# Kernel tuning notes

Hardware: AMD Instinct MI355X
Metric: run time of the kernel (lower is better)

## Reference

```python
import jax, jax.numpy as jnp
import numpy as np

N, NFEAT, OUT, NREL = 4096, 128, 64, 7


def setup_inputs() -> dict:
    key = jax.random.key(0)
    ks = jax.random.split(key, 12)
    mask = jax.random.uniform(ks[0], (NREL, N, N)) < 0.01
    vals = jax.random.uniform(ks[1], (NREL, N, N))
    A_stack = jnp.where(mask, vals, 0.0).astype(jnp.float32)
    feature = jax.random.normal(ks[2], (N, NFEAT), jnp.float32)
    encode = (jax.random.uniform(ks[3], (N, NREL)) < 0.3).astype(jnp.float32)
    stdv = 1.0 / np.sqrt(OUT)
    W1 = jax.random.uniform(ks[4], (NFEAT, OUT), jnp.float32, -stdv, stdv)
    b1 = jax.random.uniform(ks[5], (OUT,), jnp.float32, -stdv, stdv)
    W2 = jax.random.uniform(ks[6], (OUT, OUT), jnp.float32, -stdv, stdv)
    b2 = jax.random.uniform(ks[7], (OUT,), jnp.float32, -stdv, stdv)
    weight_b = jax.random.uniform(ks[8], (NREL, 1), jnp.float32, 0.0, 0.1)
    relation_interaction = 0.1 * jax.random.normal(ks[9], (3, 3), jnp.float32)
    interaction_strength = jnp.array([0.5], jnp.float32)
    struct_weight = jax.random.uniform(ks[10], (NREL,), jnp.float32, 0.0, 0.1)
    return dict(feature=feature, A_stack=A_stack, encode=encode, W1=W1, b1=b1,
                W2=W2, b2=b2, weight_b=weight_b,
                relation_interaction=relation_interaction,
                interaction_strength=interaction_strength,
                struct_weight=struct_weight)


def _l2_normalize(x):
    norm = jnp.clip(jnp.linalg.norm(x, axis=1, keepdims=True), 1e-12)
    return x / norm


def _gcn(x, adj, W, b):
    # torch.mm(input, weight) then torch.spmm(adj, support) + bias
    return adj @ (x @ W) + b


def reference(feature, A_stack, encode, W1, b1, W2, b2, weight_b,
              relation_interaction, interaction_strength, struct_weight):
    # adj_matrix_weight_merge: weighted sum of 7 relation adjacencies, symmetrized
    merged = jnp.einsum('rnm,r->nm', A_stack, weight_b[:, 0])  # [N,N]
    bbp_A = merged + merged.T

    # relation-interaction enhancement over the first 3 relations (i != j)
    R = A_stack[:3]  # [3,N,N]
    M = relation_interaction * (1.0 - jnp.eye(3, dtype=relation_interaction.dtype))
    mult = jnp.einsum('ij,inm,jnm->nm', M, R, R)                       # coeff*Ri*Rj
    cond = jnp.einsum('ij,inm,jnm->nm', M, (R > 0).astype(R.dtype), R)  # coeff*(Ri>0)*Rj
    interaction_A = jnp.tanh(0.6 * mult + 0.4 * cond)

    final_A = bbp_A + interaction_strength[0] * interaction_A

    U1 = _gcn(feature, final_A, W1, b1)
    U2 = _gcn(U1, final_A, W2, b2)

    # construct_adj(encode, struct_weight): weighted structural similarity
    struct_adj = (encode * struct_weight) @ encode.T  # [N,N]
    U3 = _gcn(feature, struct_adj, W1, b1)
    U4 = _gcn(U3, struct_adj, W2, b2)

    branch1 = (U1 + U2) / 2
    result = (branch1 + U4) / 2
    branch2 = U4
    return (_l2_normalize(result), _l2_normalize(branch1), _l2_normalize(branch2))
```

## Files before the change

kernel.cpp:

```cpp
#include <hip/hip_runtime.h>
#include <math.h>

#define NDIM 4096
#define NNSZ ((size_t)NDIM*(size_t)NDIM)
#define SCAP 262144u

typedef __attribute__((ext_vector_type(8))) short short8;
typedef __attribute__((ext_vector_type(4))) float f32x4;

__device__ __forceinline__ unsigned short f2bf(float x) {
  unsigned u = __float_as_uint(x);
  u += 0x7FFFu + ((u >> 16) & 1u);
  return (unsigned short)(u >> 16);
}
__device__ __forceinline__ float bf2f(unsigned short u) {
  return __uint_as_float(((unsigned)u) << 16);
}

__device__ __forceinline__ float inter_term(float r0, float r1, float r2,
    float m01, float m02, float m10, float m12, float m20, float m21) {
  float mult = (m01 + m10) * (r0 * r1) + (m02 + m20) * (r0 * r2) + (m12 + m21) * (r1 * r2);
  float i0 = (r0 > 0.f) ? 1.f : 0.f;
  float i1 = (r1 > 0.f) ? 1.f : 0.f;
  float i2 = (r2 > 0.f) ? 1.f : 0.f;
  float cond = m01 * i0 * r1 + m02 * i0 * r2
             + m10 * i1 * r0 + m12 * i1 * r2
             + m20 * i2 * r0 + m21 * i2 * r1;
  float a = 0.6f * mult + 0.4f * cond;
  return (a == 0.0f) ? 0.0f : tanhf(a);
}

__global__ __launch_bounds__(256, 4) void k_pass1(
    const float* __restrict__ A, const float* __restrict__ wb,
    const float* __restrict__ Mri, const float* __restrict__ strength,
    unsigned short* __restrict__ Mm, unsigned* __restrict__ sidx,
    float* __restrict__ sval, unsigned* __restrict__ scnt)
{
  const unsigned gid = blockIdx.x * 256 + threadIdx.x;
  const size_t off = (size_t)gid * 4;

  float w[7];
#pragma unroll
  for (int r = 0; r < 7; ++r) w[r] = wb[r];
  const float m01 = Mri[1], m02 = Mri[2], m10 = Mri[3];
  const float m12 = Mri[5], m20 = Mri[6], m21 = Mri[7];
  const float s = strength[0];

  float4 v[7];
#pragma unroll
  for (int r = 0; r < 7; ++r)
    v[r] = *(const float4*)(A + (size_t)r * NNSZ + off);

  float4 acc = make_float4(0.f, 0.f, 0.f, 0.f);
#pragma unroll
  for (int r = 0; r < 7; ++r) {
    acc.x = fmaf(w[r], v[r].x, acc.x);
    acc.y = fmaf(w[r], v[r].y, acc.y);
    acc.z = fmaf(w[r], v[r].z, acc.z);
    acc.w = fmaf(w[r], v[r].w, acc.w);
  }
  *(ushort4*)(Mm + off) = make_ushort4(f2bf(acc.x), f2bf(acc.y), f2bf(acc.z), f2bf(acc.w));

  {
    float r0 = v[0].x, r1 = v[1].x, r2 = v[2].x;
    if ((int)(r0 != 0.f) + (int)(r1 != 0.f) + (int)(r2 != 0.f) >= 2) {
      float t = inter_term(r0, r1, r2, m01, m02, m10, m12, m20, m21);
      unsigned idx = atomicAdd(scnt, 1u);
      if (idx < SCAP) { sidx[idx] = (unsigned)(off + 0); sval[idx] = s * t; }
    }
  }
  {
    float r0 = v[0].y, r1 = v[1].y, r2 = v[2].y;
    if ((int)(r0 != 0.f) + (int)(r1 != 0.f) + (int)(r2 != 0.f) >= 2) {
      float t = inter_term(r0, r1, r2, m01, m02, m10, m12, m20, m21);
      unsigned idx = atomicAdd(scnt, 1u);
      if (idx < SCAP) { sidx[idx] = (unsigned)(off + 1); sval[idx] = s * t; }
    }
  }
  {
    float r0 = v[0].z, r1 = v[1].z, r2 = v[2].z;
    if ((int)(r0 != 0.f) + (int)(r1 != 0.f) + (int)(r2 != 0.f) >= 2) {
      float t = inter_term(r0, r1, r2, m01, m02, m10, m12, m20, m21);
      unsigned idx = atomicAdd(scnt, 1u);
      if (idx < SCAP) { sidx[idx] = (unsigned)(off + 2); sval[idx] = s * t; }
    }
  }
  {
    float r0 = v[0].w, r1 = v[1].w, r2 = v[2].w;
    if ((int)(r0 != 0.f) + (int)(r1 != 0.f) + (int)(r2 != 0.f) >= 2) {
      float t = inter_term(r0, r1, r2, m01, m02, m10, m12, m20, m21);
      unsigned idx = atomicAdd(scnt, 1u);
      if (idx < SCAP) { sidx[idx] = (unsigned)(off + 3); sval[idx] = s * t; }
    }
  }
}

__global__ __launch_bounds__(256) void k_pass2(
    const unsigned short* __restrict__ Mm, unsigned short* __restrict__ F)
{
  const int bi = blockIdx.x, bj = blockIdx.y;
  __shared__ unsigned short t[64 * 65];
  const int x  = threadIdx.x >> 2;
  const int y0 = (threadIdx.x & 3) << 4;

  const size_t moff = (size_t)(bj * 64 + x) * NDIM + bi * 64 + y0;
  unsigned short mv[16];
  ((uint4*)mv)[0] = *(const uint4*)(Mm + moff);
  ((uint4*)mv)[1] = *(const uint4*)(Mm + moff + 8);
#pragma unroll
  for (int e = 0; e < 16; ++e) t[x * 65 + y0 + e] = mv[e];
  __syncthreads();

  const size_t off = (size_t)(bi * 64 + x) * NDIM + bj * 64 + y0;
  unsigned short pv[16], ov[16];
  ((uint4*)pv)[0] = *(const uint4*)(Mm + off);
  ((uint4*)pv)[1] = *(const uint4*)(Mm + off + 8);
#pragma unroll
  for (int e = 0; e < 16; ++e)
    ov[e] = f2bf(bf2f(pv[e]) + bf2f(t[(y0 + e) * 65 + x]));
  *(uint4*)(F + off)     = ((const uint4*)ov)[0];
  *(uint4*)(F + off + 8) = ((const uint4*)ov)[1];
}

__global__ __launch_bounds__(256) void k_fix(const unsigned* __restrict__ sidx,
    const float* __restrict__ sval, const unsigned* __restrict__ scnt,
    unsigned short* __restrict__ F) {
  unsigned n = *scnt;
  if (n > SCAP) n = SCAP;
  for (unsigned i = blockIdx.x * 256 + threadIdx.x; i < n; i += gridDim.x * 256) {
    unsigned pos = sidx[i];
    F[pos] = f2bf(bf2f(F[pos]) + sval[i]);
  }
}

__global__ __launch_bounds__(64) void k_z1(const float* __restrict__ feat,
    const float* __restrict__ W1, float* __restrict__ Z1) {
  int n = blockIdx.x, j = threadIdx.x;
  __shared__ float fr[128];
  fr[j] = feat[n * 128 + j];
  fr[j + 64] = feat[n * 128 + 64 + j];
  __syncthreads();
  float acc = 0.f;
#pragma unroll 8
  for (int k = 0; k < 128; ++k) acc = fmaf(fr[k], W1[k * 64 + j], acc);
  Z1[(size_t)n * 64 + j] = acc;
}

__global__ __launch_bounds__(256) void k_transpose_bf16(
    const float* __restrict__ Z, unsigned short* __restrict__ Zt) {
  __shared__ float tile[64][65];
  const int n0 = blockIdx.x * 64;
  const int c = threadIdx.x & 63;
  const int r0 = threadIdx.x >> 6;
#pragma unroll
  for (int i = 0; i < 16; ++i) {
    int r = r0 * 16 + i;
    tile[r][c] = Z[(size_t)(n0 + r) * 64 + c];
  }
  __syncthreads();
#pragma unroll
  for (int i = 0; i < 16; ++i) {
    int j = r0 * 16 + i;
    Zt[(size_t)j * NDIM + n0 + c] = f2bf(tile[c][j]);
  }
}

__global__ __launch_bounds__(512) void k_mfma_gemm(
    const unsigned short* __restrict__ Fb,
    const unsigned short* __restrict__ Zt,
    const float* __restrict__ bias,
    float* __restrict__ U)
{
  __shared__ float red[8][16][66];
  const int strip = blockIdx.x * 16;
  const int w = threadIdx.x >> 6;
  const int lane = threadIdx.x & 63;
  const int arow = lane & 15;
  const int kq = lane >> 4;
  const int k_base = w * 512;

  f32x4 acc[4] = {};
  const unsigned short* Ap  = Fb + (size_t)(strip + arow) * NDIM + k_base + kq * 8;
  const unsigned short* Bp0 = Zt + (size_t)(arow) * NDIM + k_base + kq * 8;
  const unsigned short* Bp1 = Bp0 + (size_t)16 * NDIM;
  const unsigned short* Bp2 = Bp0 + (size_t)32 * NDIM;
  const unsigned short* Bp3 = Bp0 + (size_t)48 * NDIM;

#pragma unroll 4
  for (int step = 0; step < 16; ++step) {
    const int k0 = step * 32;
    short8 a  = *(const short8*)(Ap  + k0);
    short8 b0 = *(const short8*)(Bp0 + k0);
    short8 b1v = *(const short8*)(Bp1 + k0);
    short8 b2v = *(const short8*)(Bp2 + k0);
    short8 b3v = *(const short8*)(Bp3 + k0);
    acc[0] = __builtin_amdgcn_mfma_f32_16x16x32_bf16(a, b0,  acc[0], 0, 0, 0);
    acc[1] = __builtin_amdgcn_mfma_f32_16x16x32_bf16(a, b1v, acc[1], 0, 0, 0);
    acc[2] = __builtin_amdgcn_mfma_f32_16x16x32_bf16(a, b2v, acc[2], 0, 0, 0);
    acc[3] = __builtin_amdgcn_mfma_f32_16x16x32_bf16(a, b3v, acc[3], 0, 0, 0);
  }
#pragma unroll
  for (int t = 0; t < 4; ++t)
#pragma unroll
    for (int r = 0; r < 4; ++r)
      red[w][kq * 4 + r][t * 16 + arow] = acc[t][r];
  __syncthreads();

  const int col = threadIdx.x & 63;
  const int row0 = threadIdx.x >> 6;
#pragma unroll
  for (int rr = 0; rr < 2; ++rr) {
    const int row = row0 + rr * 8;
    float sum = 0.f;
#pragma unroll
    for (int ww = 0; ww < 8; ++ww) sum += red[ww][row][col];
    U[(size_t)(strip + row) * 64 + col] = sum + bias[col];
  }
}

__device__ __forceinline__ float wave_sum64(float v) {
#pragma unroll
  for (int o = 32; o > 0; o >>= 1) v += __shfl_xor(v, o, 64);
  return v;
}

__global__ __launch_bounds__(512) void k_gemm2f(
    const unsigned short* __restrict__ Fb,
    const unsigned short* __restrict__ Zt,
    const float* __restrict__ b2,
    const float* __restrict__ U1,
    const float* __restrict__ encode,
    const float* __restrict__ sw,
    const float* __restrict__ G2,
    float* __restrict__ out)
{
  __shared__ float red[8][16][66];
  const int strip = blockIdx.x * 16;
  const int w = threadIdx.x >> 6;
  const int lane = threadIdx.x & 63;
  const int arow = lane & 15;
  const int kq = lane >> 4;
  const int k_base = w * 512;

  f32x4 acc[4] = {};
  const unsigned short* Ap  = Fb + (size_t)(strip + arow) * NDIM + k_base + kq * 8;
  const unsigned short* Bp0 = Zt + (size_t)(arow) * NDIM + k_base + kq * 8;
  const unsigned short* Bp1 = Bp0 + (size_t)16 * NDIM;
  const unsigned short* Bp2 = Bp0 + (size_t)32 * NDIM;
  const unsigned short* Bp3 = Bp0 + (size_t)48 * NDIM;

#pragma unroll 4
  for (int step = 0; step < 16; ++step) {
    const int k0 = step * 32;
    short8 a  = *(const short8*)(Ap  + k0);
    short8 b0 = *(const short8*)(Bp0 + k0);
    short8 b1v = *(const short8*)(Bp1 + k0);
    short8 b2v = *(const short8*)(Bp2 + k0);
    short8 b3v = *(const short8*)(Bp3 + k0);
    acc[0] = __builtin_amdgcn_mfma_f32_16x16x32_bf16(a, b0,  acc[0], 0, 0, 0);
    acc[1] = __builtin_amdgcn_mfma_f32_16x16x32_bf16(a, b1v, acc[1], 0, 0, 0);
    acc[2] = __builtin_amdgcn_mfma_f32_16x16x32_bf16(a, b2v, acc[2], 0, 0, 0);
    acc[3] = __builtin_amdgcn_mfma_f32_16x16x32_bf16(a, b3v, acc[3], 0, 0, 0);
  }
#pragma unroll
  for (int t = 0; t < 4; ++t)
#pragma unroll
    for (int r = 0; r < 4; ++r)
      red[w][kq * 4 + r][t * 16 + arow] = acc[t][r];
  __syncthreads();

  const int col = threadIdx.x & 63;
  const int row0 = threadIdx.x >> 6;
#pragma unroll
  for (int rr = 0; rr < 2; ++rr) {
    const int row = row0 + rr * 8;
    const int n = strip + row;
    float sum = 0.f;
#pragma unroll
    for (int ww = 0; ww < 8; ++ww) sum += red[ww][row][col];
    float u2 = sum + b2[col];
    float u1 = U1[(size_t)n * 64 + col];
    float br = 0.5f * (u1 + u2);
    float u4 = b2[col];
#pragma unroll
    for (int r = 0; r < 7; ++r)
      u4 = fmaf(encode[n * 7 + r] * sw[r], G2[r * 64 + col], u4);
    float rs = 0.5f * (br + u4);
    float nr = fmaxf(sqrtf(wave_sum64(rs * rs)), 1e-12f);
    float nb = fmaxf(sqrtf(wave_sum64(br * br)), 1e-12f);
    float nu = fmaxf(sqrtf(wave_sum64(u4 * u4)), 1e-12f);
    size_t idx = (size_t)n * 64 + col;
    out[idx] = rs / nr;
    out[(size_t)NDIM * 64 + idx] = br / nb;
    out[2 * (size_t)NDIM * 64 + idx] = u4 / nu;
  }
}

__global__ __launch_bounds__(256) void k_z2t(const float* __restrict__ U1,
    const float* __restrict__ W2, unsigned short* __restrict__ Z2t) {
  __shared__ float W2s[64][65];
  const int n0 = blockIdx.x * 64;
  const int j = threadIdx.x & 63;
  const int g = threadIdx.x >> 6;
  for (int r = g; r < 64; r += 4) W2s[r][j] = W2[r * 64 + j];
  __syncthreads();
  float acc[16];
#pragma unroll
  for (int r = 0; r < 16; ++r) acc[r] = 0.f;
  const float* Urow = U1 + (size_t)(n0 + g * 16) * 64;
  for (int k = 0; k < 64; ++k) {
    float wv = W2s[k][j];
#pragma unroll
    for (int r = 0; r < 16; ++r) acc[r] = fmaf(Urow[r * 64 + k], wv, acc[r]);
  }
  unsigned short ov[16];
#pragma unroll
  for (int r = 0; r < 16; ++r) ov[r] = f2bf(acc[r]);
  *(uint4*)(Z2t + (size_t)j * NDIM + n0 + g * 16)     = *(const uint4*)&ov[0];
  *(uint4*)(Z2t + (size_t)j * NDIM + n0 + g * 16 + 8) = *(const uint4*)&ov[8];
}

__global__ __launch_bounds__(512) void k_zero_small(float* __restrict__ g,
    unsigned* __restrict__ scnt) {
  int t = threadIdx.x;
  if (t < 448) g[t] = 0.f;
  if (t == 448) *scnt = 0u;
}

__global__ __launch_bounds__(256) void k_sc(const float* __restrict__ encode,
    const float* __restrict__ sw, float* __restrict__ S, float* __restrict__ c) {
  __shared__ float red[4][56];
  float sl[49], cl[7];
#pragma unroll
  for (int i = 0; i < 49; ++i) sl[i] = 0.f;
#pragma unroll
  for (int i = 0; i < 7; ++i) cl[i] = 0.f;
  for (int n = threadIdx.x; n < NDIM; n += 256) {
    float e[7];
#pragma unroll
    for (int r = 0; r < 7; ++r) e[r] = encode[n * 7 + r];
#pragma unroll
    for (int i = 0; i < 7; ++i) {
      cl[i] += e[i];
#pragma unroll
      for (int j = 0; j < 7; ++j) sl[i * 7 + j] = fmaf(e[i], e[j], sl[i * 7 + j]);
    }
  }
  const int lane = threadIdx.x & 63;
  const int w = threadIdx.x >> 6;
#pragma unroll
  for (int i = 0; i < 49; ++i) {
#pragma unroll
    for (int o = 32; o > 0; o >>= 1) sl[i] += __shfl_xor(sl[i], o, 64);
  }
#pragma unroll
  for (int i = 0; i < 7; ++i) {
#pragma unroll
    for (int o = 32; o > 0; o >>= 1) cl[i] += __shfl_xor(cl[i], o, 64);
  }
  if (lane == 0) {
#pragma unroll
    for (int i = 0; i < 49; ++i) red[w][i] = sl[i];
#pragma unroll
    for (int i = 0; i < 7; ++i) red[w][49 + i] = cl[i];
  }
  __syncthreads();
  if (threadIdx.x < 49)
    S[threadIdx.x] = (red[0][threadIdx.x] + red[1][threadIdx.x] + red[2][threadIdx.x] + red[3][threadIdx.x]) * sw[threadIdx.x % 7];
  if (threadIdx.x >= 49 && threadIdx.x < 56) {
    int i = threadIdx.x;
    c[i - 49] = red[0][i] + red[1][i] + red[2][i] + red[3][i];
  }
}

__global__ __launch_bounds__(256) void k_g1(const float* __restrict__ encode,
    const float* __restrict__ Z1, float* __restrict__ G1) {
  const int j = threadIdx.x & 63;
  const int grp = threadIdx.x >> 6;
  const int n0 = blockIdx.x * 128 + grp * 32;
  float acc[7];
#pragma unroll
  for (int r = 0; r < 7; ++r) acc[r] = 0.f;
  for (int i = 0; i < 32; ++i) {
    int n = n0 + i;
    float z = Z1[(size_t)n * 64 + j];
#pragma unroll
    for (int r = 0; r < 7; ++r) acc[r] = fmaf(encode[n * 7 + r], z, acc[r]);
  }
#pragma unroll
  for (int r = 0; r < 7; ++r) atomicAdd(&G1[r * 64 + j], acc[r]);
}

__global__ __launch_bounds__(64) void k_g2(const float* __restrict__ S,
    const float* __restrict__ c, const float* __restrict__ G1,
    const float* __restrict__ W2, const float* __restrict__ b1,
    float* __restrict__ G2) {
  int j = threadIdx.x;
  float h = 0.f;
  for (int k = 0; k < 64; ++k) h = fmaf(b1[k], W2[k * 64 + j], h);
  float gw[7];
#pragma unroll
  for (int r = 0; r < 7; ++r) {
    float v = 0.f;
    for (int k = 0; k < 64; ++k) v = fmaf(G1[r * 64 + k], W2[k * 64 + j], v);
    gw[r] = v;
  }
#pragma unroll
  for (int r = 0; r < 7; ++r) {
    float v = c[r] * h;
#pragma unroll
    for (int q = 0; q < 7; ++q) v = fmaf(S[r * 7 + q], gw[q], v);
    G2[r * 64 + j] = v;
  }
}

extern "C" void kernel_launch(void* const* d_in, const int* in_sizes, int n_in,
                              void* d_out, int out_size, void* d_ws, size_t ws_size,
                              hipStream_t stream) {
  const float* feature  = (const float*)d_in[0];
  const float* A        = (const float*)d_in[1];
  const float* encode   = (const float*)d_in[2];
  const float* W1       = (const float*)d_in[3];
  const float* b1       = (const float*)d_in[4];
  const float* W2       = (const float*)d_in[5];
  const float* b2       = (const float*)d_in[6];
  const float* wb       = (const float*)d_in[7];
  const float* Mri      = (const float*)d_in[8];
  const float* strength = (const float*)d_in[9];
  const float* sw       = (const float*)d_in[10];
  float* out = (float*)d_out;

  const size_t NV = (size_t)NDIM * 64;
  unsigned* sidx = (unsigned*)d_ws;
  float* sval = (float*)(sidx + SCAP);
  unsigned* scnt = (unsigned*)(sval + SCAP);
  unsigned short* Mm = (unsigned short*)d_ws + NNSZ;
  unsigned short* Fb = Mm + NNSZ;
  float* Z1 = (float*)(Fb + NNSZ);
  float* U1 = Z1 + NV;
  float* U2 = U1 + NV;
  unsigned short* Z1t = (unsigned short*)(U2 + NV);
  unsigned short* Z2t = Z1t + NV;
  float* G1 = (float*)(Z2t + NV);
  float* S  = G1 + 448;
  float* c  = S + 49;
  float* G2 = c + 7;

  hipLaunchKernelGGL(k_zero_small, dim3(1), dim3(512), 0, stream, G1, scnt);
  hipLaunchKernelGGL(k_pass1, dim3(16384), dim3(256), 0, stream, A, wb, Mri, strength, Mm, sidx, sval, scnt);
  hipLaunchKernelGGL(k_pass2, dim3(64, 64), dim3(256), 0, stream, Mm, Fb);
  hipLaunchKernelGGL(k_fix, dim3(32), dim3(256), 0, stream, sidx, sval, scnt, Fb);
  hipLaunchKernelGGL(k_z1, dim3(NDIM), dim3(64), 0, stream, feature, W1, Z1);
  hipLaunchKernelGGL(k_transpose_bf16, dim3(64), dim3(256), 0, stream, Z1, Z1t);
  hipLaunchKernelGGL(k_sc, dim3(1), dim3(256), 0, stream, encode, sw, S, c);
  hipLaunchKernelGGL(k_g1, dim3(32), dim3(256), 0, stream, encode, Z1, G1);
  hipLaunchKernelGGL(k_g2, dim3(1), dim3(64), 0, stream, S, c, G1, W2, b1, G2);
  hipLaunchKernelGGL(k_mfma_gemm, dim3(NDIM / 16), dim3(512), 0, stream, Fb, Z1t, b1, U1);
  hipLaunchKernelGGL(k_z2t, dim3(64), dim3(256), 0, stream, U1, W2, Z2t);
  hipLaunchKernelGGL(k_gemm2f, dim3(NDIM / 16), dim3(512), 0, stream, Fb, Z2t, b2, U1, encode, sw, G2, out);
}
```

Baseline: 238.0 us.

## Fuse feature projection with transpose and restructure structural-branch reductions

Merges the per-row feature×W1 projection and the bf16 transpose into one tiled kernel that writes Z1t directly, dropping the fp32 Z1 buffer. The structural-branch precomputation is reassociated to reduce encodeᵀ·feature (EF) first, then apply W1 inside the small G2 kernel. The S/c reduction moves from a single block to 16 blocks with atomics. This cuts five small launches to three and removes a round trip through global memory. In exchange the project kernel runs only 64 blocks, and atomic accumulation makes the float sums order-dependent.

```diff
diff --git a/kernel.cpp b/kernel.cpp
--- a/kernel.cpp
+++ b/kernel.cpp
@@ -133,35 +133,121 @@
   }
 }
 
-__global__ __launch_bounds__(64) void k_z1(const float* __restrict__ feat,
-    const float* __restrict__ W1, float* __restrict__ Z1) {
-  int n = blockIdx.x, j = threadIdx.x;
-  __shared__ float fr[128];
-  fr[j] = feat[n * 128 + j];
-  fr[j + 64] = feat[n * 128 + 64 + j];
-  __syncthreads();
-  float acc = 0.f;
-#pragma unroll 8
-  for (int k = 0; k < 128; ++k) acc = fmaf(fr[k], W1[k * 64 + j], acc);
-  Z1[(size_t)n * 64 + j] = acc;
-}
-
-__global__ __launch_bounds__(256) void k_transpose_bf16(
-    const float* __restrict__ Z, unsigned short* __restrict__ Zt) {
-  __shared__ float tile[64][65];
+__global__ __launch_bounds__(256) void k_z1t2(const float* __restrict__ feat,
+    const float* __restrict__ W1, unsigned short* __restrict__ Z1t) {
+  __shared__ float ftile[64][129];
   const int n0 = blockIdx.x * 64;
-  const int c = threadIdx.x & 63;
-  const int r0 = threadIdx.x >> 6;
-#pragma unroll
-  for (int i = 0; i < 16; ++i) {
-    int r = r0 * 16 + i;
-    tile[r][c] = Z[(size_t)(n0 + r) * 64 + c];
-  }
-  __syncthreads();
-#pragma unroll
-  for (int i = 0; i < 16; ++i) {
-    int j = r0 * 16 + i;
-    Zt[(size_t)j * NDIM + n0 + c] = f2bf(tile[c][j]);
+#pragma unroll
+  for (int i = 0; i < 32; ++i) {
+    int idx = i * 256 + threadIdx.x;
+    int r = idx >> 7, cc = idx & 127;
+    ftile[r][cc] = feat[(size_t)(n0 + r) * 128 + cc];
+  }
+  __syncthreads();
+
+  const int j = threadIdx.x & 63;
+  const int g = threadIdx.x >> 6;
+  float acc[16];
+#pragma unroll
+  for (int i = 0; i < 16; ++i) acc[i] = 0.f;
+  for (int k = 0; k < 128; ++k) {
+    float wv = W1[k * 64 + j];
+#pragma unroll
+    for (int i = 0; i < 16; ++i)
+      acc[i] = fmaf(ftile[g * 16 + i][k], wv, acc[i]);
+  }
+  unsigned short ov[16];
+#pragma unroll
+  for (int i = 0; i < 16; ++i) ov[i] = f2bf(acc[i]);
+  *(uint4*)(Z1t + (size_t)j * NDIM + n0 + g * 16)     = ((const uint4*)ov)[0];
+  *(uint4*)(Z1t + (size_t)j * NDIM + n0 + g * 16 + 8) = ((const uint4*)ov)[1];
+}
+
+__global__ __launch_bounds__(256) void k_scef(const float* __restrict__ encode,
+    const float* __restrict__ feat, float* __restrict__ EF,
+    float* __restrict__ Sraw, float* __restrict__ craw) {
+  const int base = blockIdx.x * 256;
+  const int tid = threadIdx.x;
+  __shared__ float enc[256 * 7];
+  __shared__ float red[4][56];
+  __shared__ float efred[7][128];
+  for (int i = tid; i < 256 * 7; i += 256) enc[i] = encode[(size_t)base * 7 + i];
+  __syncthreads();
+
+  float e[7];
+#pragma unroll
+  for (int r = 0; r < 7; ++r) e[r] = enc[tid * 7 + r];
+  float sl[56];
+#pragma unroll
+  for (int i = 0; i < 7; ++i)
+#pragma unroll
+    for (int j2 = 0; j2 < 7; ++j2) sl[i * 7 + j2] = e[i] * e[j2];
+#pragma unroll
+  for (int i = 0; i < 7; ++i) sl[49 + i] = e[i];
+  const int lane = tid & 63, w = tid >> 6;
+#pragma unroll
+  for (int i = 0; i < 56; ++i) {
+#pragma unroll
+    for (int o = 32; o > 0; o >>= 1) sl[i] += __shfl_xor(sl[i], o, 64);
+  }
+  if (lane == 0) {
+#pragma unroll
+    for (int i = 0; i < 56; ++i) red[w][i] = sl[i];
+  }
+  __syncthreads();
+  if (tid < 56) {
+    float v = red[0][tid] + red[1][tid] + red[2][tid] + red[3][tid];
+    if (tid < 49) atomicAdd(&Sraw[tid], v);
+    else          atomicAdd(&craw[tid - 49], v);
+  }
+
+  float ef[7] = {0.f, 0.f, 0.f, 0.f, 0.f, 0.f, 0.f};
+  const int cc = tid & 127, half = tid >> 7;
+  for (int nl = half * 128; nl < half * 128 + 128; ++nl) {
+    float fv = feat[(size_t)(base + nl) * 128 + cc];
+#pragma unroll
+    for (int r = 0; r < 7; ++r) ef[r] = fmaf(enc[nl * 7 + r], fv, ef[r]);
+  }
+  if (half == 0) {
+#pragma unroll
+    for (int r = 0; r < 7; ++r) efred[r][cc] = ef[r];
+  }
+  __syncthreads();
+  if (half == 1) {
+#pragma unroll
+    for (int r = 0; r < 7; ++r) atomicAdd(&EF[r * 128 + cc], efred[r][cc] + ef[r]);
+  }
+}
+
+__global__ __launch_bounds__(64) void k_g2v2(const float* __restrict__ Sraw,
+    const float* __restrict__ sw, const float* __restrict__ craw,
+    const float* __restrict__ EF, const float* __restrict__ W1,
+    const float* __restrict__ W2, const float* __restrict__ b1,
+    float* __restrict__ G2) {
+  __shared__ float G1s[7][64];
+  const int j = threadIdx.x;
+#pragma unroll
+  for (int r = 0; r < 7; ++r) {
+    float v = 0.f;
+    for (int k = 0; k < 128; ++k) v = fmaf(EF[r * 128 + k], W1[k * 64 + j], v);
+    G1s[r][j] = v;
+  }
+  __syncthreads();
+  float h = 0.f;
+  for (int k = 0; k < 64; ++k) h = fmaf(b1[k], W2[k * 64 + j], h);
+  float gw[7];
+#pragma unroll
+  for (int r = 0; r < 7; ++r) {
+    float v = 0.f;
+    for (int k = 0; k < 64; ++k) v = fmaf(G1s[r][k], W2[k * 64 + j], v);
+    gw[r] = v;
+  }
+#pragma unroll
+  for (int r = 0; r < 7; ++r) {
+    float v = craw[r] * h;
+#pragma unroll
+    for (int q = 0; q < 7; ++q) v = fmaf(Sraw[r * 7 + q] * sw[q], gw[q], v);
+    G2[r * 64 + j] = v;
   }
 }
 
@@ -323,95 +409,9 @@
 __global__ __launch_bounds__(512) void k_zero_small(float* __restrict__ g,
     unsigned* __restrict__ scnt) {
   int t = threadIdx.x;
-  if (t < 448) g[t] = 0.f;
-  if (t == 448) *scnt = 0u;
-}
-
-__global__ __launch_bounds__(256) void k_sc(const float* __restrict__ encode,
-    const float* __restrict__ sw, float* __restrict__ S, float* __restrict__ c) {
-  __shared__ float red[4][56];
-  float sl[49], cl[7];
-#pragma unroll
-  for (int i = 0; i < 49; ++i) sl[i] = 0.f;
-#pragma unroll
-  for (int i = 0; i < 7; ++i) cl[i] = 0.f;
-  for (int n = threadIdx.x; n < NDIM; n += 256) {
-    float e[7];
-#pragma unroll
-    for (int r = 0; r < 7; ++r) e[r] = encode[n * 7 + r];
-#pragma unroll
-    for (int i = 0; i < 7; ++i) {
-      cl[i] += e[i];
-#pragma unroll
-      for (int j = 0; j < 7; ++j) sl[i * 7 + j] = fmaf(e[i], e[j], sl[i * 7 + j]);
-    }
-  }
-  const int lane = threadIdx.x & 63;
-  const int w = threadIdx.x >> 6;
-#pragma unroll
-  for (int i = 0; i < 49; ++i) {
-#pragma unroll
-    for (int o = 32; o > 0; o >>= 1) sl[i] += __shfl_xor(sl[i], o, 64);
-  }
-#pragma unroll
-  for (int i = 0; i < 7; ++i) {
-#pragma unroll
-    for (int o = 32; o > 0; o >>= 1) cl[i] += __shfl_xor(cl[i], o, 64);
-  }
-  if (lane == 0) {
-#pragma unroll
-    for (int i = 0; i < 49; ++i) red[w][i] = sl[i];
-#pragma unroll
-    for (int i = 0; i < 7; ++i) red[w][49 + i] = cl[i];
-  }
-  __syncthreads();
-  if (threadIdx.x < 49)
-    S[threadIdx.x] = (red[0][threadIdx.x] + red[1][threadIdx.x] + red[2][threadIdx.x] + red[3][threadIdx.x]) * sw[threadIdx.x % 7];
-  if (threadIdx.x >= 49 && threadIdx.x < 56) {
-    int i = threadIdx.x;
-    c[i - 49] = red[0][i] + red[1][i] + red[2][i] + red[3][i];
-  }
-}
-
-__global__ __launch_bounds__(256) void k_g1(const float* __restrict__ encode,
-    const float* __restrict__ Z1, float* __restrict__ G1) {
-  const int j = threadIdx.x & 63;
-  const int grp = threadIdx.x >> 6;
-  const int n0 = blockIdx.x * 128 + grp * 32;
-  float acc[7];
-#pragma unroll
-  for (int r = 0; r < 7; ++r) acc[r] = 0.f;
-  for (int i = 0; i < 32; ++i) {
-    int n = n0 + i;
-    float z = Z1[(size_t)n * 64 + j];
-#pragma unroll
-    for (int r = 0; r < 7; ++r) acc[r] = fmaf(encode[n * 7 + r], z, acc[r]);
-  }
-#pragma unroll
-  for (int r = 0; r < 7; ++r) atomicAdd(&G1[r * 64 + j], acc[r]);
-}
-
-__global__ __launch_bounds__(64) void k_g2(const float* __restrict__ S,
-    const float* __restrict__ c, const float* __restrict__ G1,
-    const float* __restrict__ W2, const float* __restrict__ b1,
-    float* __restrict__ G2) {
-  int j = threadIdx.x;
-  float h = 0.f;
-  for (int k = 0; k < 64; ++k) h = fmaf(b1[k], W2[k * 64 + j], h);
-  float gw[7];
-#pragma unroll
-  for (int r = 0; r < 7; ++r) {
-    float v = 0.f;
-    for (int k = 0; k < 64; ++k) v = fmaf(G1[r * 64 + k], W2[k * 64 + j], v);
-    gw[r] = v;
-  }
-#pragma unroll
-  for (int r = 0; r < 7; ++r) {
-    float v = c[r] * h;
-#pragma unroll
-    for (int q = 0; q < 7; ++q) v = fmaf(S[r * 7 + q], gw[q], v);
-    G2[r * 64 + j] = v;
-  }
+#pragma unroll
+  for (int i = 0; i < 2; ++i) g[t + i * 512] = 0.f;
+  if (t == 0) *scnt = 0u;
 }
 
 extern "C" void kernel_launch(void* const* d_in, const int* in_sizes, int n_in,
@@ -436,25 +436,22 @@
   unsigned* scnt = (unsigned*)(sval + SCAP);
   unsigned short* Mm = (unsigned short*)d_ws + NNSZ;
   unsigned short* Fb = Mm + NNSZ;
-  float* Z1 = (float*)(Fb + NNSZ);
-  float* U1 = Z1 + NV;
-  float* U2 = U1 + NV;
-  unsigned short* Z1t = (unsigned short*)(U2 + NV);
+  float* U1 = (float*)(Fb + NNSZ);
+  unsigned short* Z1t = (unsigned short*)(U1 + NV);
   unsigned short* Z2t = Z1t + NV;
-  float* G1 = (float*)(Z2t + NV);
-  float* S  = G1 + 448;
-  float* c  = S + 49;
-  float* G2 = c + 7;
-
-  hipLaunchKernelGGL(k_zero_small, dim3(1), dim3(512), 0, stream, G1, scnt);
+  float* smallb = (float*)(Z2t + NV);
+  float* EF   = smallb;
+  float* Sraw = smallb + 896;
+  float* craw = smallb + 945;
+  float* G2   = smallb + 952;
+
+  hipLaunchKernelGGL(k_zero_small, dim3(1), dim3(512), 0, stream, smallb, scnt);
   hipLaunchKernelGGL(k_pass1, dim3(16384), dim3(256), 0, stream, A, wb, Mri, strength, Mm, sidx, sval, scnt);
   hipLaunchKernelGGL(k_pass2, dim3(64, 64), dim3(256), 0, stream, Mm, Fb);
   hipLaunchKernelGGL(k_fix, dim3(32), dim3(256), 0, stream, sidx, sval, scnt, Fb);
-  hipLaunchKernelGGL(k_z1, dim3(NDIM), dim3(64), 0, stream, feature, W1, Z1);
-  hipLaunchKernelGGL(k_transpose_bf16, dim3(64), dim3(256), 0, stream, Z1, Z1t);
-  hipLaunchKernelGGL(k_sc, dim3(1), dim3(256), 0, stream, encode, sw, S, c);
-  hipLaunchKernelGGL(k_g1, dim3(32), dim3(256), 0, stream, encode, Z1, G1);
-  hipLaunchKernelGGL(k_g2, dim3(1), dim3(64), 0, stream, S, c, G1, W2, b1, G2);
+  hipLaunchKernelGGL(k_z1t2, dim3(64), dim3(256), 0, stream, feature, W1, Z1t);
+  hipLaunchKernelGGL(k_scef, dim3(16), dim3(256), 0, stream, encode, feature, EF, Sraw, craw);
+  hipLaunchKernelGGL(k_g2v2, dim3(1), dim3(64), 0, stream, Sraw, sw, craw, EF, W1, W2, b1, G2);
   hipLaunchKernelGGL(k_mfma_gemm, dim3(NDIM / 16), dim3(512), 0, stream, Fb, Z1t, b1, U1);
   hipLaunchKernelGGL(k_z2t, dim3(64), dim3(256), 0, stream, U1, W2, Z2t);
   hipLaunchKernelGGL(k_gemm2f, dim3(NDIM / 16), dim3(512), 0, stream, Fb, Z2t, b2, U1, encode, sw, G2, out);
```

Result: slower. 273.3 us (+14.8%).
